# Optimization experiments

Measured on AMD Instinct MI355X. Metric: run time of the kernel, lower is better.

## Reference

```python
import jax, jax.numpy as jnp
import numpy as np

B, D, H, OUT = 16384, 4096, 7, 7


def setup_inputs() -> dict:
    key = jax.random.key(0)
    k1, k2, k3, k4 = jax.random.split(key, 4)
    features1 = jax.random.normal(k1, (B, D), dtype=jnp.float32)
    features2 = jax.random.normal(k2, (B, D), dtype=jnp.float32)
    W1 = jax.random.normal(k3, (D, H), dtype=jnp.float32) * (1.0 / np.sqrt(D))
    b1 = jnp.zeros((H,), dtype=jnp.float32)
    W2 = jax.random.normal(k4, (H, OUT), dtype=jnp.float32) * (1.0 / np.sqrt(H))
    b2 = jnp.zeros((OUT,), dtype=jnp.float32)
    return {"features1": features1, "features2": features2,
            "W1": W1, "b1": b1, "W2": W2, "b2": b2}


def reference(features1, features2, W1, b1, W2, b2):
    # Gate MLP (Dropout is inference-mode identity): [B, D] -> [B, 7]
    def mlp(x):
        h = jax.nn.relu(x @ W1 + b1)
        return h @ W2 + b2

    # Per-sample scalar logit for each expert: mean over the 7 gate outputs.
    logit1 = mlp(features1).mean(axis=1)  # [B]
    logit2 = mlp(features2).mean(axis=1)  # [B]

    # Per-sample softmax over the 2 experts (vectorized form of the batch loop).
    alpha = jax.nn.softmax(jnp.stack([logit1, logit2], axis=1), axis=1)  # [B, 2]

    # Weighted 2-expert combine: alpha0 * f1 + alpha1 * f2, shape [B, D].
    return alpha[:, 0:1] * features1 + alpha[:, 1:2] * features2
```

## Files before the change

kernel.cpp:

```cpp
#include <hip/hip_runtime.h>
#include <hip/hip_bf16.h>


constexpr int Dk  = 4096;
constexpr int Hk  = 7;
constexpr int NPAIR = Dk / 512;
constexpr int NWE   = Hk * NPAIR * 64;
constexpr int WPK_WORDS = NWE * 4;
constexpr size_t WS_NEEDED = (size_t)WPK_WORDS * 4 + 64;

constexpr int NTH = 1024;
constexpr int ROWS_PER_BLOCK = 4;

__global__ void gating_prep(const float* __restrict__ W1,
                            const float* __restrict__ b1,
                            const float* __restrict__ W2,
                            const float* __restrict__ b2,
                            unsigned int* __restrict__ wsw)
{
    const int t = blockIdx.x * blockDim.x + threadIdx.x;
    if (t < NWE) {
        const int j    = t / (NPAIR * 64);
        const int kk   = (t / 64) % NPAIR;
        const int lane = t & 63;
        const int vi0  = (2 * kk) * 64 + lane;
        unsigned int w[4];
        #pragma unroll
        for (int h = 0; h < 2; ++h) {
            const int vi = vi0 + h * 64;
            #pragma unroll
            for (int p = 0; p < 2; ++p) {
                const int d0 = 4 * vi + 2 * p;
                const unsigned int lo = (unsigned int)__bfloat16_as_ushort(
                    __float2bfloat16(W1[(long long)d0 * Hk + j]));
                const unsigned int hi = (unsigned int)__bfloat16_as_ushort(
                    __float2bfloat16(W1[(long long)(d0 + 1) * Hk + j]));
                w[h * 2 + p] = lo | (hi << 16);
            }
        }
        reinterpret_cast<uint4*>(wsw)[t] = make_uint4(w[0], w[1], w[2], w[3]);
    }
    if (blockIdx.x == 0 && threadIdx.x == 0) {
        float* c = reinterpret_cast<float*>(wsw) + WPK_WORDS;
        #pragma unroll
        for (int j = 0; j < Hk; ++j) {
            c[j] = b1[j];
            float s = 0.f;
            #pragma unroll
            for (int k = 0; k < Hk; ++k) s += W2[j * Hk + k];
            c[Hk + j] = s;
        }
        float sb2 = 0.f;
        #pragma unroll
        for (int k = 0; k < Hk; ++k) sb2 += b2[k];
        c[14] = sb2;
    }
}

__device__ __forceinline__ float bf_lo(unsigned int u) {
    return __uint_as_float(u << 16);
}
__device__ __forceinline__ float bf_hi(unsigned int u) {
    return __uint_as_float(u & 0xFFFF0000u);
}

__global__ __launch_bounds__(NTH, 8)
void gating_wave(const float* __restrict__ f1,
                 const float* __restrict__ f2,
                 const uint4* __restrict__ wpk,
                 const float* __restrict__ gc,
                 float* __restrict__ out,
                 int rows)
{
    __shared__ uint4 wl[NWE];
    __shared__ float red[ROWS_PER_BLOCK][2][Hk][4];

    for (int e = threadIdx.x; e < NWE; e += NTH)
        wl[e] = wpk[e];
    __syncthreads();

    const int wid  = threadIdx.x >> 6;
    const int lane = threadIdx.x & 63;
    const int lrow = wid >> 2;
    const int q    = wid & 3;
    int row = blockIdx.x * ROWS_PER_BLOCK + lrow;
    if (row >= rows) row = rows - 1;

    const long long base = (long long)row * Dk;
    const float4* __restrict__ f1v = reinterpret_cast<const float4*>(f1 + base);
    const float4* __restrict__ f2v = reinterpret_cast<const float4*>(f2 + base);

    float4 a[4], b[4];
    #pragma unroll
    for (int i = 0; i < 4; ++i) {
        const int vi = (4 * q + i) * 64 + lane;
        a[i] = f1v[vi];
        b[i] = f2v[vi];
    }
    __builtin_amdgcn_sched_barrier(0);

    float acc1[Hk], acc2[Hk];
    #pragma unroll
    for (int j = 0; j < Hk; ++j) { acc1[j] = 0.f; acc2[j] = 0.f; }

    #pragma unroll
    for (int kk2 = 0; kk2 < 2; ++kk2) {
        const int kk = 2 * q + kk2;
        const float4 xa0 = a[2 * kk2],     xb0 = b[2 * kk2];
        const float4 xa1 = a[2 * kk2 + 1], xb1 = b[2 * kk2 + 1];
        #pragma unroll
        for (int j = 0; j < Hk; ++j) {
            const uint4 u = wl[(j * NPAIR + kk) * 64 + lane];
            const float w0 = bf_lo(u.x), w1 = bf_hi(u.x);
            const float w2 = bf_lo(u.y), w3 = bf_hi(u.y);
            const float w4 = bf_lo(u.z), w5 = bf_hi(u.z);
            const float w6 = bf_lo(u.w), w7 = bf_hi(u.w);
            acc1[j] = fmaf(xa0.x, w0, fmaf(xa0.y, w1,
                      fmaf(xa0.z, w2, fmaf(xa0.w, w3, acc1[j]))));
            acc1[j] = fmaf(xa1.x, w4, fmaf(xa1.y, w5,
                      fmaf(xa1.z, w6, fmaf(xa1.w, w7, acc1[j]))));
            acc2[j] = fmaf(xb0.x, w0, fmaf(xb0.y, w1,
                      fmaf(xb0.z, w2, fmaf(xb0.w, w3, acc2[j]))));
            acc2[j] = fmaf(xb1.x, w4, fmaf(xb1.y, w5,
                      fmaf(xb1.z, w6, fmaf(xb1.w, w7, acc2[j]))));
        }
    }

    #pragma unroll
    for (int j = 0; j < Hk; ++j) {
        acc1[j] += __shfl_xor(acc1[j], 32);
        acc2[j] += __shfl_xor(acc2[j], 32);
    }
    float val[Hk];
    #pragma unroll
    for (int j = 0; j < Hk; ++j)
        val[j] = (lane < 32) ? acc1[j] : acc2[j];
    #pragma unroll
    for (int off = 16; off >= 1; off >>= 1) {
        #pragma unroll
        for (int j = 0; j < Hk; ++j)
            val[j] += __shfl_xor(val[j], off);
    }

    if ((lane & 31) == 0) {
        const int e = lane >> 5;
        #pragma unroll
        for (int j = 0; j < Hk; ++j)
            red[lrow][e][j][q] = val[j];
    }
    __syncthreads();

    float l1 = 0.f, l2 = 0.f;
    #pragma unroll
    for (int j = 0; j < Hk; ++j) {
        const float4 r1q = *reinterpret_cast<const float4*>(&red[lrow][0][j][0]);
        const float4 r2q = *reinterpret_cast<const float4*>(&red[lrow][1][j][0]);
        const float h1 = r1q.x + r1q.y + r1q.z + r1q.w + gc[j];
        const float h2 = r2q.x + r2q.y + r2q.z + r2q.w + gc[j];
        l1 = fmaf(fmaxf(h1, 0.f), gc[Hk + j], l1);
        l2 = fmaf(fmaxf(h2, 0.f), gc[Hk + j], l2);
    }
    const float delta = (l2 - l1) * (1.f / 7.f);
    const float a0 = 1.f / (1.f + expf(delta));
    const float a1 = 1.f - a0;

    float4* __restrict__ ov = reinterpret_cast<float4*>(out + base);
    #pragma unroll
    for (int i = 0; i < 4; ++i) {
        const int vi = (4 * q + i) * 64 + lane;
        float4 o;
        o.x = fmaf(a0, a[i].x, a1 * b[i].x);
        o.y = fmaf(a0, a[i].y, a1 * b[i].y);
        o.z = fmaf(a0, a[i].z, a1 * b[i].z);
        o.w = fmaf(a0, a[i].w, a1 * b[i].w);
        ov[vi] = o;
    }
}

__global__ __launch_bounds__(256, 4)
void gating_fused_direct(const float* __restrict__ f1,
                         const float* __restrict__ f2,
                         const float* __restrict__ W1,
                         const float* __restrict__ b1,
                         const float* __restrict__ W2,
                         const float* __restrict__ b2,
                         float* __restrict__ out)
{
    constexpr int VPT = 4;
    const int row = blockIdx.x;
    const int t   = threadIdx.x;
    const long long base = (long long)row * Dk;

    const float4* f1v = reinterpret_cast<const float4*>(f1 + base);
    const float4* f2v = reinterpret_cast<const float4*>(f2 + base);

    float4 r1[VPT], r2[VPT];
    float acc1[Hk], acc2[Hk];
    #pragma unroll
    for (int j = 0; j < Hk; ++j) { acc1[j] = 0.f; acc2[j] = 0.f; }

    #pragma unroll
    for (int k = 0; k < VPT; ++k) {
        const int vi = k * 256 + t;
        r1[k] = f1v[vi];
        r2[k] = f2v[vi];
        const float4* wv = reinterpret_cast<const float4*>(W1 + (long long)vi * 28);
        float4 w4[7];
        #pragma unroll
        for (int q = 0; q < 7; ++q) w4[q] = wv[q];
        const float* ws = reinterpret_cast<const float*>(w4);
        const float* x1 = reinterpret_cast<const float*>(&r1[k]);
        const float* x2 = reinterpret_cast<const float*>(&r2[k]);
        #pragma unroll
        for (int r = 0; r < 4; ++r)
            #pragma unroll
            for (int j = 0; j < Hk; ++j) {
                acc1[j] = fmaf(x1[r], ws[r * 7 + j], acc1[j]);
                acc2[j] = fmaf(x2[r], ws[r * 7 + j], acc2[j]);
            }
    }
    #pragma unroll
    for (int j = 0; j < Hk; ++j)
        #pragma unroll
        for (int off = 32; off >= 1; off >>= 1) {
            acc1[j] += __shfl_down(acc1[j], off);
            acc2[j] += __shfl_down(acc2[j], off);
        }

    __shared__ float red[4][2 * Hk];
    __shared__ float alpha[2];
    const int wave = t >> 6;
    const int lane = t & 63;
    if (lane == 0)
        #pragma unroll
        for (int j = 0; j < Hk; ++j) {
            red[wave][j]      = acc1[j];
            red[wave][Hk + j] = acc2[j];
        }
    __syncthreads();

    if (t == 0) {
        float l1 = 0.f, l2 = 0.f;
        #pragma unroll
        for (int j = 0; j < Hk; ++j) {
            float h1 = red[0][j] + red[1][j] + red[2][j] + red[3][j] + b1[j];
            float h2 = red[0][Hk + j] + red[1][Hk + j] + red[2][Hk + j]
                     + red[3][Hk + j] + b1[j];
            float s = 0.f;
            #pragma unroll
            for (int k2 = 0; k2 < Hk; ++k2) s += W2[j * Hk + k2];
            l1 = fmaf(fmaxf(h1, 0.f), s, l1);
            l2 = fmaf(fmaxf(h2, 0.f), s, l2);
        }
        float sb2 = 0.f;
        #pragma unroll
        for (int k2 = 0; k2 < Hk; ++k2) sb2 += b2[k2];
        l1 = (l1 + sb2) * (1.f / 7.f);
        l2 = (l2 + sb2) * (1.f / 7.f);
        const float a0 = 1.f / (1.f + expf(l2 - l1));
        alpha[0] = a0;
        alpha[1] = 1.f - a0;
    }
    __syncthreads();

    const float a0 = alpha[0];
    const float a1 = alpha[1];
    float4* ov = reinterpret_cast<float4*>(out + base);
    #pragma unroll
    for (int k = 0; k < VPT; ++k) {
        const int vi = k * 256 + t;
        float4 o;
        o.x = a0 * r1[k].x + a1 * r2[k].x;
        o.y = a0 * r1[k].y + a1 * r2[k].y;
        o.z = a0 * r1[k].z + a1 * r2[k].z;
        o.w = a0 * r1[k].w + a1 * r2[k].w;
        ov[vi] = o;
    }
}

extern "C" void kernel_launch(void* const* d_in, const int* in_sizes, int n_in,
                              void* d_out, int out_size, void* d_ws, size_t ws_size,
                              hipStream_t stream) {
    const float* f1 = (const float*)d_in[0];
    const float* f2 = (const float*)d_in[1];
    const float* W1 = (const float*)d_in[2];
    const float* b1 = (const float*)d_in[3];
    const float* W2 = (const float*)d_in[4];
    const float* b2 = (const float*)d_in[5];
    float* out = (float*)d_out;
    const int rows = in_sizes[0] / Dk;

    if (ws_size >= WS_NEEDED) {
        unsigned int* wsw = (unsigned int*)d_ws;
        gating_prep<<<(NWE + 255) / 256, 256, 0, stream>>>(W1, b1, W2, b2, wsw);
        const int blocks = (rows + ROWS_PER_BLOCK - 1) / ROWS_PER_BLOCK;
        gating_wave<<<blocks, NTH, 0, stream>>>(
            f1, f2, reinterpret_cast<const uint4*>(wsw),
            reinterpret_cast<const float*>(wsw) + WPK_WORDS, out, rows);
    } else {
        gating_fused_direct<<<rows, 256, 0, stream>>>(f1, f2, W1, b1, W2, b2, out);
    }
}
```

Baseline: 164.3 us.

## Make gating kernel persistent with grid-stride row sets

```diff
diff --git a/kernel.cpp b/kernel.cpp
--- a/kernel.cpp
+++ b/kernel.cpp
@@ -9,8 +9,9 @@
 constexpr int WPK_WORDS = NWE * 4;
 constexpr size_t WS_NEEDED = (size_t)WPK_WORDS * 4 + 64;
 
-constexpr int NTH = 1024;
-constexpr int ROWS_PER_BLOCK = 4;
+constexpr int NTH  = 1024;
+constexpr int NBLK = 512;
+constexpr int ROWS_PER_SET = 4;
 
 __global__ void gating_prep(const float* __restrict__ W1,
                             const float* __restrict__ b1,
@@ -73,7 +74,7 @@
                  int rows)
 {
     __shared__ uint4 wl[NWE];
-    __shared__ float red[ROWS_PER_BLOCK][2][Hk][4];
+    __shared__ float red[2][ROWS_PER_SET][2][Hk][4];
 
     for (int e = threadIdx.x; e < NWE; e += NTH)
         wl[e] = wpk[e];
@@ -83,97 +84,107 @@
     const int lane = threadIdx.x & 63;
     const int lrow = wid >> 2;
     const int q    = wid & 3;
-    int row = blockIdx.x * ROWS_PER_BLOCK + lrow;
-    if (row >= rows) row = rows - 1;
-
-    const long long base = (long long)row * Dk;
-    const float4* __restrict__ f1v = reinterpret_cast<const float4*>(f1 + base);
-    const float4* __restrict__ f2v = reinterpret_cast<const float4*>(f2 + base);
-
-    float4 a[4], b[4];
-    #pragma unroll
-    for (int i = 0; i < 4; ++i) {
-        const int vi = (4 * q + i) * 64 + lane;
-        a[i] = f1v[vi];
-        b[i] = f2v[vi];
-    }
-    __builtin_amdgcn_sched_barrier(0);
-
-    float acc1[Hk], acc2[Hk];
-    #pragma unroll
-    for (int j = 0; j < Hk; ++j) { acc1[j] = 0.f; acc2[j] = 0.f; }
-
-    #pragma unroll
-    for (int kk2 = 0; kk2 < 2; ++kk2) {
-        const int kk = 2 * q + kk2;
-        const float4 xa0 = a[2 * kk2],     xb0 = b[2 * kk2];
-        const float4 xa1 = a[2 * kk2 + 1], xb1 = b[2 * kk2 + 1];
-        #pragma unroll
-        for (int j = 0; j < Hk; ++j) {
-            const uint4 u = wl[(j * NPAIR + kk) * 64 + lane];
-            const float w0 = bf_lo(u.x), w1 = bf_hi(u.x);
-            const float w2 = bf_lo(u.y), w3 = bf_hi(u.y);
-            const float w4 = bf_lo(u.z), w5 = bf_hi(u.z);
-            const float w6 = bf_lo(u.w), w7 = bf_hi(u.w);
-            acc1[j] = fmaf(xa0.x, w0, fmaf(xa0.y, w1,
-                      fmaf(xa0.z, w2, fmaf(xa0.w, w3, acc1[j]))));
-            acc1[j] = fmaf(xa1.x, w4, fmaf(xa1.y, w5,
-                      fmaf(xa1.z, w6, fmaf(xa1.w, w7, acc1[j]))));
-            acc2[j] = fmaf(xb0.x, w0, fmaf(xb0.y, w1,
-                      fmaf(xb0.z, w2, fmaf(xb0.w, w3, acc2[j]))));
-            acc2[j] = fmaf(xb1.x, w4, fmaf(xb1.y, w5,
-                      fmaf(xb1.z, w6, fmaf(xb1.w, w7, acc2[j]))));
-        }
-    }
-
-    #pragma unroll
-    for (int j = 0; j < Hk; ++j) {
-        acc1[j] += __shfl_xor(acc1[j], 32);
-        acc2[j] += __shfl_xor(acc2[j], 32);
-    }
-    float val[Hk];
-    #pragma unroll
-    for (int j = 0; j < Hk; ++j)
-        val[j] = (lane < 32) ? acc1[j] : acc2[j];
-    #pragma unroll
-    for (int off = 16; off >= 1; off >>= 1) {
+
+    float b1r[Hk], sr[Hk];
+    #pragma unroll
+    for (int j = 0; j < Hk; ++j) { b1r[j] = gc[j]; sr[j] = gc[Hk + j]; }
+
+    const int nrowsets = (rows + ROWS_PER_SET - 1) / ROWS_PER_SET;
+    int p = 0;
+
+    for (int rs = blockIdx.x; rs < nrowsets; rs += gridDim.x, p ^= 1) {
+        int row = rs * ROWS_PER_SET + lrow;
+        if (row >= rows) row = rows - 1;
+
+        const long long base = (long long)row * Dk;
+        const float4* __restrict__ f1v = reinterpret_cast<const float4*>(f1 + base);
+        const float4* __restrict__ f2v = reinterpret_cast<const float4*>(f2 + base);
+
+        float4 a[4], b[4];
+        #pragma unroll
+        for (int i = 0; i < 4; ++i) {
+            const int vi = (4 * q + i) * 64 + lane;
+            a[i] = f1v[vi];
+            b[i] = f2v[vi];
+        }
+        __builtin_amdgcn_sched_barrier(0);
+
+        float acc1[Hk], acc2[Hk];
+        #pragma unroll
+        for (int j = 0; j < Hk; ++j) { acc1[j] = 0.f; acc2[j] = 0.f; }
+
+        #pragma unroll
+        for (int kk2 = 0; kk2 < 2; ++kk2) {
+            const int kk = 2 * q + kk2;
+            const float4 xa0 = a[2 * kk2],     xb0 = b[2 * kk2];
+            const float4 xa1 = a[2 * kk2 + 1], xb1 = b[2 * kk2 + 1];
+            #pragma unroll
+            for (int j = 0; j < Hk; ++j) {
+                const uint4 u = wl[(j * NPAIR + kk) * 64 + lane];
+                const float w0 = bf_lo(u.x), w1 = bf_hi(u.x);
+                const float w2 = bf_lo(u.y), w3 = bf_hi(u.y);
+                const float w4 = bf_lo(u.z), w5 = bf_hi(u.z);
+                const float w6 = bf_lo(u.w), w7 = bf_hi(u.w);
+                acc1[j] = fmaf(xa0.x, w0, fmaf(xa0.y, w1,
+                          fmaf(xa0.z, w2, fmaf(xa0.w, w3, acc1[j]))));
+                acc1[j] = fmaf(xa1.x, w4, fmaf(xa1.y, w5,
+                          fmaf(xa1.z, w6, fmaf(xa1.w, w7, acc1[j]))));
+                acc2[j] = fmaf(xb0.x, w0, fmaf(xb0.y, w1,
+                          fmaf(xb0.z, w2, fmaf(xb0.w, w3, acc2[j]))));
+                acc2[j] = fmaf(xb1.x, w4, fmaf(xb1.y, w5,
+                          fmaf(xb1.z, w6, fmaf(xb1.w, w7, acc2[j]))));
+            }
+        }
+
+        #pragma unroll
+        for (int j = 0; j < Hk; ++j) {
+            acc1[j] += __shfl_xor(acc1[j], 32);
+            acc2[j] += __shfl_xor(acc2[j], 32);
+        }
+        float val[Hk];
         #pragma unroll
         for (int j = 0; j < Hk; ++j)
-            val[j] += __shfl_xor(val[j], off);
-    }
-
-    if ((lane & 31) == 0) {
-        const int e = lane >> 5;
-        #pragma unroll
-        for (int j = 0; j < Hk; ++j)
-            red[lrow][e][j][q] = val[j];
-    }
-    __syncthreads();
-
-    float l1 = 0.f, l2 = 0.f;
-    #pragma unroll
-    for (int j = 0; j < Hk; ++j) {
-        const float4 r1q = *reinterpret_cast<const float4*>(&red[lrow][0][j][0]);
-        const float4 r2q = *reinterpret_cast<const float4*>(&red[lrow][1][j][0]);
-        const float h1 = r1q.x + r1q.y + r1q.z + r1q.w + gc[j];
-        const float h2 = r2q.x + r2q.y + r2q.z + r2q.w + gc[j];
-        l1 = fmaf(fmaxf(h1, 0.f), gc[Hk + j], l1);
-        l2 = fmaf(fmaxf(h2, 0.f), gc[Hk + j], l2);
-    }
-    const float delta = (l2 - l1) * (1.f / 7.f);
-    const float a0 = 1.f / (1.f + expf(delta));
-    const float a1 = 1.f - a0;
-
-    float4* __restrict__ ov = reinterpret_cast<float4*>(out + base);
-    #pragma unroll
-    for (int i = 0; i < 4; ++i) {
-        const int vi = (4 * q + i) * 64 + lane;
-        float4 o;
-        o.x = fmaf(a0, a[i].x, a1 * b[i].x);
-        o.y = fmaf(a0, a[i].y, a1 * b[i].y);
-        o.z = fmaf(a0, a[i].z, a1 * b[i].z);
-        o.w = fmaf(a0, a[i].w, a1 * b[i].w);
-        ov[vi] = o;
+            val[j] = (lane < 32) ? acc1[j] : acc2[j];
+        #pragma unroll
+        for (int off = 16; off >= 1; off >>= 1) {
+            #pragma unroll
+            for (int j = 0; j < Hk; ++j)
+                val[j] += __shfl_xor(val[j], off);
+        }
+
+        if ((lane & 31) == 0) {
+            const int e = lane >> 5;
+            #pragma unroll
+            for (int j = 0; j < Hk; ++j)
+                red[p][lrow][e][j][q] = val[j];
+        }
+        __syncthreads();
+
+        float l1 = 0.f, l2 = 0.f;
+        #pragma unroll
+        for (int j = 0; j < Hk; ++j) {
+            const float4 r1q = *reinterpret_cast<const float4*>(&red[p][lrow][0][j][0]);
+            const float4 r2q = *reinterpret_cast<const float4*>(&red[p][lrow][1][j][0]);
+            const float h1 = r1q.x + r1q.y + r1q.z + r1q.w + b1r[j];
+            const float h2 = r2q.x + r2q.y + r2q.z + r2q.w + b1r[j];
+            l1 = fmaf(fmaxf(h1, 0.f), sr[j], l1);
+            l2 = fmaf(fmaxf(h2, 0.f), sr[j], l2);
+        }
+        const float delta = (l2 - l1) * (1.f / 7.f);
+        const float a0 = 1.f / (1.f + expf(delta));
+        const float a1 = 1.f - a0;
+
+        float4* __restrict__ ov = reinterpret_cast<float4*>(out + base);
+        #pragma unroll
+        for (int i = 0; i < 4; ++i) {
+            const int vi = (4 * q + i) * 64 + lane;
+            float4 o;
+            o.x = fmaf(a0, a[i].x, a1 * b[i].x);
+            o.y = fmaf(a0, a[i].y, a1 * b[i].y);
+            o.z = fmaf(a0, a[i].z, a1 * b[i].z);
+            o.w = fmaf(a0, a[i].w, a1 * b[i].w);
+            ov[vi] = o;
+        }
     }
 }
 
@@ -293,8 +304,7 @@
     if (ws_size >= WS_NEEDED) {
         unsigned int* wsw = (unsigned int*)d_ws;
         gating_prep<<<(NWE + 255) / 256, 256, 0, stream>>>(W1, b1, W2, b2, wsw);
-        const int blocks = (rows + ROWS_PER_BLOCK - 1) / ROWS_PER_BLOCK;
-        gating_wave<<<blocks, NTH, 0, stream>>>(
+        gating_wave<<<NBLK, NTH, 0, stream>>>(
             f1, f2, reinterpret_cast<const uint4*>(wsw),
             reinterpret_cast<const float*>(wsw) + WPK_WORDS, out, rows);
     } else {
```

Result: slower. 169.6 us (+3.2%).
